# Performance work log

Hardware: AMD Instinct MI355X
Metric: run time of the kernel (lower is better)

## Reference

```python
import jax, jax.numpy as jnp
import numpy as np

N_LINEARS = 16
CHANNELS = 3
OUTPUT_DIM = 64
Z_DIM = 128
BATCH = 512


def hash_vectors(z, n):
    # Deterministic surrogate for repo's hash_vectors: map each latent vector
    # to an integer bucket in [0, n). Data-dependent, jit-compatible.
    s = jnp.abs(jnp.sum(z, axis=1)) * 1000.0
    return jnp.mod(jnp.floor(s).astype(jnp.int32), n)


def setup_inputs() -> dict:
    key = jax.random.key(0)
    k1, k2, k3 = jax.random.split(key, 3)
    out_features = CHANNELS * OUTPUT_DIM ** 2 * N_LINEARS  # 196608
    z = jax.random.normal(k1, (BATCH, Z_DIM), dtype=jnp.float32)
    # Linear weight stored as (out_features, in_features), torch convention.
    W = jax.random.normal(k2, (out_features, Z_DIM), dtype=jnp.float32) * (1.0 / np.sqrt(Z_DIM))
    b = jax.random.normal(k3, (out_features,), dtype=jnp.float32) * 0.01
    return {"z": z, "W": W, "b": b}


def reference(z, W, b):
    B = z.shape[0]
    # Dense GEMM: (B, out_features)
    out = jnp.einsum('bi,oi->bo', z, W) + b
    out = out.reshape(B, N_LINEARS, CHANNELS, OUTPUT_DIM, OUTPUT_DIM)
    c = hash_vectors(z, N_LINEARS)  # (B,) int32 in [0, N_LINEARS)
    # Per-sample gather of one linear's output block.
    return jnp.take_along_axis(out, c[:, None, None, None, None], axis=1)[:, 0]
```

## Files before the change

### kernel.cpp

```cpp
#include <hip/hip_runtime.h>
#include <hip/hip_bf16.h>
#include <math.h>


#define N_LINEARS 16
#define ZD 128
#define BATCH 512
#define BLOCK_OUT 12288
#define STILE 32
#define SLOTS 64
#define ZROWS (ZD + 1)
#define TJ 256

#define ZG_OFF_BYTES 65536
#define ZG_FLOATS (N_LINEARS * ZROWS * SLOTS)

__global__ __launch_bounds__(128) void hash_gather_kernel(
    const float* __restrict__ z, int* __restrict__ counts,
    int* __restrict__ lists, float* __restrict__ zgT) {
  const int b = blockIdx.x;
  const int tid = threadIdx.x;
  const float* zr = z + b * ZD;

  __shared__ int sh_c, sh_pos;

  if (tid < 8) {
    float r = zr[tid];
    #pragma unroll
    for (int i = 8; i < ZD; i += 8) r += zr[i + tid];
    float t1 = r + __shfl_down(r, 1, 64);
    float t2 = t1 + __shfl_down(t1, 2, 64);
    float res = t2 + __shfl_down(t2, 4, 64);
    if (tid == 0) {
      float v = fabsf(res) * 1000.0f;
      int cb = ((int)floorf(v)) & (N_LINEARS - 1);
      int pos = atomicAdd(&counts[cb], 1);
      if (pos < SLOTS) lists[(cb << 9) + pos] = b;
      sh_c = cb; sh_pos = pos;
    }
  }
  __syncthreads();
  const int c = sh_c, pos = sh_pos;
  if (pos < SLOTS) {
    zgT[(size_t)c * (ZROWS * SLOTS) + (size_t)tid * SLOTS + pos] = zr[tid];
  }
}


#define ZLOAD(NXT, K1)                                              \
  { const float4* zrow_ = (const float4*)(ztp + (size_t)(K1) * SLOTS); \
    _Pragma("unroll")                                               \
    for (int q = 0; q < 8; ++q) NXT[q] = zrow_[q]; }

#define ZFMA(CUR, WK)                                               \
  { const float wk_ = (WK);                                         \
    _Pragma("unroll")                                               \
    for (int q = 0; q < 8; ++q) {                                   \
      acc[4*q+0] = fmaf(wk_, CUR[q].x, acc[4*q+0]);                 \
      acc[4*q+1] = fmaf(wk_, CUR[q].y, acc[4*q+1]);                 \
      acc[4*q+2] = fmaf(wk_, CUR[q].z, acc[4*q+2]);                 \
      acc[4*q+3] = fmaf(wk_, CUR[q].w, acc[4*q+3]); } }

#define STEP(CUR, NXT, K1, WK) ZLOAD(NXT, K1) ZFMA(CUR, WK)

__global__ __launch_bounds__(TJ, 3) void gen_main_kernel(
    const float* __restrict__ W, const float* __restrict__ bias,
    float* __restrict__ out, const int* __restrict__ counts,
    const int* __restrict__ lists, const float* __restrict__ zgT) {
  const int c = blockIdx.y;
  const int j = blockIdx.x * TJ + threadIdx.x;
  int n = counts[c];
  n = n > SLOTS ? SLOTS : n;
  if (n == 0) return;

  const size_t row = (size_t)c * BLOCK_OUT + (size_t)j;
  const float4* __restrict__ Wv = (const float4*)(W + row * (size_t)ZD);
  const float bj = bias[row];
  const float* __restrict__ zt = zgT + (size_t)c * (ZROWS * SLOTS);
  const int* __restrict__ lst = lists + (c << 9);

  for (int s0 = 0; s0 < n; s0 += STILE) {
    const int m = n - s0;
    float acc[STILE];
    #pragma unroll
    for (int t = 0; t < STILE; ++t) acc[t] = bj;

    const float* ztp = zt + s0;
    float4 zA[8], zB[8];
    ZLOAD(zA, 0)
    float4 wq  = Wv[0];
    float4 wqn = Wv[1];

    for (int kc = 0; kc < ZD / 4; ++kc) {
      const int k0 = kc * 4;
      STEP(zA, zB, k0 + 1, wq.x)
      STEP(zB, zA, k0 + 2, wq.y)
      STEP(zA, zB, k0 + 3, wq.z)
      STEP(zB, zA, k0 + 4, wq.w)
      wq = wqn;
      const int wi = kc + 2 > 31 ? 31 : kc + 2;
      wqn = Wv[wi];
    }

    #pragma unroll
    for (int t = 0; t < STILE; ++t) {
      if (t < m) {
        const int bs = lst[s0 + t];
        out[(size_t)bs * BLOCK_OUT + (size_t)j] = acc[t];
      }
    }
  }
}

extern "C" void kernel_launch(void* const* d_in, const int* in_sizes, int n_in,
                              void* d_out, int out_size, void* d_ws, size_t ws_size,
                              hipStream_t stream) {
  const float* z    = (const float*)d_in[0];
  const float* W    = (const float*)d_in[1];
  const float* bias = (const float*)d_in[2];
  float* out = (float*)d_out;

  int* counts = (int*)d_ws;
  int* lists  = counts + 16;
  float* zgT  = (float*)((char*)d_ws + ZG_OFF_BYTES);

  hipMemsetAsync(counts, 0, 64, stream);

  hipLaunchKernelGGL(hash_gather_kernel, dim3(BATCH), dim3(128), 0, stream,
                     z, counts, lists, zgT);

  dim3 grid(BLOCK_OUT / TJ, N_LINEARS);
  hipLaunchKernelGGL(gen_main_kernel, grid, dim3(TJ), 0, stream,
                     W, bias, out, counts, lists, zgT);
}
```

Before: 227.6 us.

## Widen sample tile to 48 with vector types and split hash/gather kernels

The sample tile per thread grows from 32 to 48, held in three 16-wide ext_vector accumulators, so a bucket of up to 48 samples needs one pass over W instead of two. The hash step becomes a single-block kernel using shared-memory atomics, which removes the memset and the global atomics; a separate gather kernel then scatters z into the transposed buffer. The cost is more accumulator and z-buffer registers, which may spill or lower occupancy under launch_bounds(256,3), plus one extra kernel launch.

Result: faster. 201.9 us (-11.3%).

```diff
diff --git a/kernel.cpp b/kernel.cpp
--- a/kernel.cpp
+++ b/kernel.cpp
@@ -7,61 +7,71 @@
 #define ZD 128
 #define BATCH 512
 #define BLOCK_OUT 12288
-#define STILE 32
+#define STILE 48
 #define SLOTS 64
 #define ZROWS (ZD + 1)
 #define TJ 256
 
+typedef float vf16 __attribute__((ext_vector_type(16)));
+typedef vf16 vf16u __attribute__((aligned(16)));
+
+#define LISTS_OFF 16
+#define BP_OFF (36864 / 4)
 #define ZG_OFF_BYTES 65536
-#define ZG_FLOATS (N_LINEARS * ZROWS * SLOTS)
 
-__global__ __launch_bounds__(128) void hash_gather_kernel(
+__global__ __launch_bounds__(512) void hash_kernel(
     const float* __restrict__ z, int* __restrict__ counts,
-    int* __restrict__ lists, float* __restrict__ zgT) {
+    int* __restrict__ lists, int* __restrict__ bp) {
+  __shared__ int cnt[N_LINEARS];
+  const int b = threadIdx.x;
+  if (b < N_LINEARS) cnt[b] = 0;
+  __syncthreads();
+
+  const float* zr = z + b * ZD;
+  float r0 = zr[0], r1 = zr[1], r2 = zr[2], r3 = zr[3];
+  float r4 = zr[4], r5 = zr[5], r6 = zr[6], r7 = zr[7];
+  #pragma unroll
+  for (int i = 8; i < ZD; i += 8) {
+    r0 += zr[i + 0]; r1 += zr[i + 1]; r2 += zr[i + 2]; r3 += zr[i + 3];
+    r4 += zr[i + 4]; r5 += zr[i + 5]; r6 += zr[i + 6]; r7 += zr[i + 7];
+  }
+  float res = ((r0 + r1) + (r2 + r3)) + ((r4 + r5) + (r6 + r7));
+  float v = fabsf(res) * 1000.0f;
+  int cb = ((int)floorf(v)) & (N_LINEARS - 1);
+
+  int pos = atomicAdd(&cnt[cb], 1);
+  lists[(cb << 9) + pos] = b;
+  bp[b] = cb | (pos << 4);
+
+  __syncthreads();
+  if (b < N_LINEARS) counts[b] = cnt[b];
+}
+
+__global__ __launch_bounds__(128) void gather_kernel(
+    const float* __restrict__ z, const int* __restrict__ bp,
+    float* __restrict__ zgT) {
   const int b = blockIdx.x;
-  const int tid = threadIdx.x;
-  const float* zr = z + b * ZD;
-
-  __shared__ int sh_c, sh_pos;
-
-  if (tid < 8) {
-    float r = zr[tid];
-    #pragma unroll
-    for (int i = 8; i < ZD; i += 8) r += zr[i + tid];
-    float t1 = r + __shfl_down(r, 1, 64);
-    float t2 = t1 + __shfl_down(t1, 2, 64);
-    float res = t2 + __shfl_down(t2, 4, 64);
-    if (tid == 0) {
-      float v = fabsf(res) * 1000.0f;
-      int cb = ((int)floorf(v)) & (N_LINEARS - 1);
-      int pos = atomicAdd(&counts[cb], 1);
-      if (pos < SLOTS) lists[(cb << 9) + pos] = b;
-      sh_c = cb; sh_pos = pos;
-    }
-  }
-  __syncthreads();
-  const int c = sh_c, pos = sh_pos;
-  if (pos < SLOTS) {
-    zgT[(size_t)c * (ZROWS * SLOTS) + (size_t)tid * SLOTS + pos] = zr[tid];
-  }
+  const int k = threadIdx.x;
+  const int v = bp[b];
+  const int cb = v & 15;
+  const int pos = v >> 4;
+  if (pos < SLOTS)
+    zgT[(size_t)cb * (ZROWS * SLOTS) + (size_t)k * SLOTS + pos] = z[b * ZD + k];
 }
 
 
-#define ZLOAD(NXT, K1)                                              \
-  { const float4* zrow_ = (const float4*)(ztp + (size_t)(K1) * SLOTS); \
-    _Pragma("unroll")                                               \
-    for (int q = 0; q < 8; ++q) NXT[q] = zrow_[q]; }
+#define ZLOAD(N0, N1, N2, K1)                                        \
+  { const vf16u* zr_ = (const vf16u*)(ztp + (size_t)(K1) * SLOTS);   \
+    N0 = zr_[0]; N1 = zr_[1]; N2 = zr_[2]; }
 
-#define ZFMA(CUR, WK)                                               \
-  { const float wk_ = (WK);                                         \
-    _Pragma("unroll")                                               \
-    for (int q = 0; q < 8; ++q) {                                   \
-      acc[4*q+0] = fmaf(wk_, CUR[q].x, acc[4*q+0]);                 \
-      acc[4*q+1] = fmaf(wk_, CUR[q].y, acc[4*q+1]);                 \
-      acc[4*q+2] = fmaf(wk_, CUR[q].z, acc[4*q+2]);                 \
-      acc[4*q+3] = fmaf(wk_, CUR[q].w, acc[4*q+3]); } }
+#define ZFMA(C0, C1, C2, WK)                                         \
+  { const float wk_ = (WK);                                          \
+    vf16 wv_;                                                        \
+    _Pragma("unroll") for (int e = 0; e < 16; ++e) wv_[e] = wk_;     \
+    acc0 += C0 * wv_; acc1 += C1 * wv_; acc2 += C2 * wv_; }
 
-#define STEP(CUR, NXT, K1, WK) ZLOAD(NXT, K1) ZFMA(CUR, WK)
+#define STEP(C0, C1, C2, N0, N1, N2, K1, WK)                         \
+  ZLOAD(N0, N1, N2, K1) ZFMA(C0, C1, C2, WK)
 
 __global__ __launch_bounds__(TJ, 3) void gen_main_kernel(
     const float* __restrict__ W, const float* __restrict__ bias,
@@ -81,34 +91,36 @@
 
   for (int s0 = 0; s0 < n; s0 += STILE) {
     const int m = n - s0;
-    float acc[STILE];
+    vf16 acc0, acc1, acc2;
     #pragma unroll
-    for (int t = 0; t < STILE; ++t) acc[t] = bj;
+    for (int e = 0; e < 16; ++e) { acc0[e] = bj; acc1[e] = bj; acc2[e] = bj; }
 
     const float* ztp = zt + s0;
-    float4 zA[8], zB[8];
-    ZLOAD(zA, 0)
+    vf16 zA0, zA1, zA2, zB0, zB1, zB2;
+    ZLOAD(zA0, zA1, zA2, 0)
     float4 wq  = Wv[0];
     float4 wqn = Wv[1];
 
     for (int kc = 0; kc < ZD / 4; ++kc) {
       const int k0 = kc * 4;
-      STEP(zA, zB, k0 + 1, wq.x)
-      STEP(zB, zA, k0 + 2, wq.y)
-      STEP(zA, zB, k0 + 3, wq.z)
-      STEP(zB, zA, k0 + 4, wq.w)
+      STEP(zA0, zA1, zA2, zB0, zB1, zB2, k0 + 1, wq.x)
+      STEP(zB0, zB1, zB2, zA0, zA1, zA2, k0 + 2, wq.y)
+      STEP(zA0, zA1, zA2, zB0, zB1, zB2, k0 + 3, wq.z)
+      STEP(zB0, zB1, zB2, zA0, zA1, zA2, k0 + 4, wq.w)
       wq = wqn;
       const int wi = kc + 2 > 31 ? 31 : kc + 2;
       wqn = Wv[wi];
     }
 
     #pragma unroll
-    for (int t = 0; t < STILE; ++t) {
-      if (t < m) {
-        const int bs = lst[s0 + t];
-        out[(size_t)bs * BLOCK_OUT + (size_t)j] = acc[t];
-      }
-    }
+    for (int t = 0; t < 16; ++t)
+      if (t < m) out[(size_t)lst[s0 + t] * BLOCK_OUT + j] = acc0[t];
+    #pragma unroll
+    for (int t = 0; t < 16; ++t)
+      if (16 + t < m) out[(size_t)lst[s0 + 16 + t] * BLOCK_OUT + j] = acc1[t];
+    #pragma unroll
+    for (int t = 0; t < 16; ++t)
+      if (32 + t < m) out[(size_t)lst[s0 + 32 + t] * BLOCK_OUT + j] = acc2[t];
   }
 }
 
@@ -120,14 +132,15 @@
   const float* bias = (const float*)d_in[2];
   float* out = (float*)d_out;
 
-  int* counts = (int*)d_ws;
-  int* lists  = counts + 16;
-  float* zgT  = (float*)((char*)d_ws + ZG_OFF_BYTES);
+  int*   counts = (int*)d_ws;
+  int*   lists  = (int*)d_ws + LISTS_OFF;
+  int*   bp     = (int*)d_ws + BP_OFF;
+  float* zgT    = (float*)((char*)d_ws + ZG_OFF_BYTES);
 
-  hipMemsetAsync(counts, 0, 64, stream);
-
-  hipLaunchKernelGGL(hash_gather_kernel, dim3(BATCH), dim3(128), 0, stream,
-                     z, counts, lists, zgT);
+  hipLaunchKernelGGL(hash_kernel, dim3(1), dim3(BATCH), 0, stream,
+                     z, counts, lists, bp);
+  hipLaunchKernelGGL(gather_kernel, dim3(BATCH), dim3(ZD), 0, stream,
+                     z, bp, zgT);
 
   dim3 grid(BLOCK_OUT / TJ, N_LINEARS);
   hipLaunchKernelGGL(gen_main_kernel, grid, dim3(TJ), 0, stream,
```
